# Kernel tuning notes

Hardware: AMD Instinct MI355X
Metric: run time of the kernel (lower is better)

## Reference

```python
import jax, jax.numpy as jnp
import numpy as np

jax.config.update("jax_enable_x64", True)  # FixedPointMul math is done in float64, as in torch

B, S, H = 8, 4096, 768


def setup_inputs():
    key = jax.random.key(0)
    k = jax.random.split(key, 6)
    s_act = jnp.array([4.0 / 127.0], dtype=jnp.float32)  # per-tensor 8-bit activation scale

    def qact(kk):  # produce int8-quantized-looking activations
        x = jax.random.normal(kk, (B, S, H), jnp.float32)
        return s_act * jnp.clip(jnp.round(x / s_act), -128, 127)

    return {
        "hidden_states": qact(k[0]),
        "hidden_states_scaling_factor": s_act,
        "input_tensor": qact(k[1]),
        "input_tensor_scaling_factor": s_act,
        "dense_weight": 0.02 * jax.random.normal(k[2], (H, H), jnp.float32),
        "dense_bias": 0.01 * jax.random.normal(k[3], (H,), jnp.float32),
        "ln_weight": 1.0 + 0.05 * jax.random.normal(k[4], (H,), jnp.float32),
        "ln_bias": 0.05 * jax.random.normal(k[5], (H,), jnp.float32),
    }


def _sym_scale(k, smin, smax):
    n = 2 ** (k - 1) - 1
    return jnp.clip(jnp.maximum(jnp.abs(smin), jnp.abs(smax)), 1e-8, None) / n


def _sym_quant(x, k, scale):
    n = 2 ** (k - 1) - 1
    return jnp.clip(jnp.round(x / scale), -n, n - 1)


def _batch_frexp(x):
    # returns (round(mantissa * 2^31), 31 - exponent) as in ibert batch_frexp
    m, e = jnp.frexp(x)
    return jnp.floor(m * (2.0 ** 31) + 0.5), 31.0 - e


def _fixedpoint_mul(x, pre_scale, bit, z_scale, identity=None, id_scale=None):
    n = 2 ** (bit - 1) - 1
    ps = jnp.reshape(pre_scale, (1, 1, -1)).astype(jnp.float64)
    z = z_scale.astype(jnp.float64)
    z_int = jnp.round(x.astype(jnp.float64) / ps)
    m, e = _batch_frexp(ps / z)
    out = jnp.round(z_int * m / (2.0 ** e))
    if identity is not None:
        isf = jnp.reshape(id_scale, (1, 1, -1)).astype(jnp.float64)
        wx = jnp.round(identity.astype(jnp.float64) / isf)
        m1, e1 = _batch_frexp(isf / z)
        out = out + jnp.round(wx * m1 / (2.0 ** e1))
    return jnp.clip(out, -n - 1, n).astype(jnp.float32)


def _quant_act(x, bit, pre_scale, identity=None, id_scale=None):
    x_act = x if identity is None else x + identity
    s = _sym_scale(bit, x_act.min(), x_act.max())  # per-tensor scale (dynamic range)
    q = _fixedpoint_mul(x, pre_scale, bit, s, identity, id_scale)
    return q * s, s


def reference(hidden_states, hidden_states_scaling_factor, input_tensor, input_tensor_scaling_factor, dense_weight, dense_bias, ln_weight, ln_bias):
    # ---- QuantLinear: per-channel int8 weights, int32 bias ----
    w_min = dense_weight.min(axis=1)
    w_max = dense_weight.max(axis=1)
    fc_scale = _sym_scale(8, w_min, w_max)                      # [H_out]
    w_int = _sym_quant(dense_weight, 8, fc_scale[:, None])      # [H_out, H_in]
    bias_scale = fc_scale * hidden_states_scaling_factor        # [H_out]
    b_int = _sym_quant(dense_bias, 32, bias_scale)
    x_int = hidden_states / hidden_states_scaling_factor
    hs = (jnp.einsum("bsh,oh->bso", x_int, w_int) + b_int) * bias_scale
    # dropout: eval mode -> identity
    # ---- QuantAct(22-bit) with quantized residual add ----
    hs, ln_in_scale = _quant_act(hs, 22, bias_scale, input_tensor, input_tensor_scaling_factor)
    # ---- IntLayerNorm (integer-only LayerNorm) ----
    x_int = hs / ln_in_scale
    mean_int = jnp.round(jnp.mean(x_int, axis=2, keepdims=True))
    y_int = x_int - mean_int
    var0 = jnp.sum(y_int ** 2, axis=2, keepdims=True)
    shift = jnp.ceil(jnp.log2(jnp.sqrt(jnp.maximum(var0, 1.0) / 2.0 ** 32)))  # set_shift (max_bit=32)
    shift = jnp.maximum(0.0, shift.max())
    y_sh = jnp.floor(y_int / 2.0 ** shift)
    var_int = jnp.sum(y_sh ** 2, axis=2, keepdims=True)
    std_int = jnp.floor(jnp.sqrt(var_int)) * 2.0 ** shift
    factor = jnp.floor(2.0 ** 31 / std_int)
    y_int = jnp.floor(y_int * factor / 2.0)
    sf = jnp.sqrt(jnp.float32(H)) / 2.0 ** 30
    bias_int = jnp.floor((ln_bias / ln_weight) / sf)
    y_int = y_int + bias_int
    sf_out = sf * ln_weight                                     # [H]
    hs = y_int * sf_out
    # ---- QuantAct(8-bit) output requantization ----
    hs, out_scale = _quant_act(hs, 8, sf_out)
    return hs, out_scale
```

## Files before the change

kernel.cpp:

```cpp
#include <hip/hip_runtime.h>

typedef int   v4i   __attribute__((ext_vector_type(4)));
typedef unsigned long u64x2 __attribute__((ext_vector_type(2)));

#define HDIM 768
#define NTOK 32768

static constexpr size_t WX_OFF   = 0;
static constexpr size_t WINT_OFF = 25165824;
static constexpr size_t FACT_OFF = WINT_OFF + 589824;
static constexpr size_t RS1_OFF  = WINT_OFF + 1179648;
static constexpr size_t RS2_OFF  = RS1_OFF + 6144;
static constexpr size_t BS_OFF   = RS2_OFF + 6144;
static constexpr size_t BINT_OFF = BS_OFF + 3072;
static constexpr size_t LNBI_OFF = BINT_OFF + 3072;
static constexpr size_t SFO_OFF  = LNBI_OFF + 3072;
static constexpr size_t SC_OFF   = SFO_OFF + 3072;
static constexpr size_t RSM1_OFF = SC_OFF + 64;
static constexpr size_t INP8_OFF = RSM1_OFF + 64;
static constexpr size_t WS_NEED8 = INP8_OFF + (size_t)NTOK * HDIM;

__device__ __forceinline__ unsigned fenc(float f) {
    unsigned u = __float_as_uint(f);
    return (u >> 31) ? ~u : (u | 0x80000000u);
}
__device__ __forceinline__ float fdec(unsigned e) {
    unsigned u = (e >> 31) ? (e & 0x7fffffffu) : ~e;
    return __uint_as_float(u);
}

#define GLDS16(g, l) __builtin_amdgcn_global_load_lds( \
    (const __attribute__((address_space(1))) unsigned int*)(g), \
    (__attribute__((address_space(3))) unsigned int*)(l), 16, 0, 0)

__device__ __forceinline__ int swz4(int r) { return (r & 3) ^ ((r >> 2) & 3); }

__global__ __launch_bounds__(256) void k0_prep(const float* __restrict__ W,
                                               const float* __restrict__ bias,
                                               const float* __restrict__ ln_w,
                                               const float* __restrict__ ln_b,
                                               const float* __restrict__ phsf,
                                               char* __restrict__ ws) {
    int o = blockIdx.x, tid = threadIdx.x;
    __shared__ float red[256];
    __shared__ float fc_sh;
    float m = 0.f;
    for (int j = tid; j < HDIM; j += 256) m = fmaxf(m, fabsf(W[(size_t)o * HDIM + j]));
    red[tid] = m;
    __syncthreads();
    for (int s = 128; s; s >>= 1) { if (tid < s) red[tid] = fmaxf(red[tid], red[tid + s]); __syncthreads(); }
    if (tid == 0) {
        float fc = fmaxf(red[0], 1e-8f) / 127.0f;
        float hsf = *phsf;
        float bs = fc * hsf;
        fc_sh = fc;
        ((float*)(ws + BS_OFF))[o] = bs;
        ((int*)(ws + BINT_OFF))[o] = (int)rintf(bias[o] / bs);
        float sf = sqrtf(768.0f) / 1073741824.0f;
        float lw = ln_w[o], lb = ln_b[o];
        ((int*)(ws + LNBI_OFF))[o] = (int)floorf((lb / lw) / sf);
        ((float*)(ws + SFO_OFF))[o] = sf * lw;
    }
    __syncthreads();
    float fc = fc_sh;
    char* w8 = (char*)(ws + WINT_OFF);
    for (int j = tid; j < HDIM; j += 256) {
        float q = rintf(W[(size_t)o * HDIM + j] / fc);
        q = fminf(fmaxf(q, -127.f), 126.f);
        w8[(size_t)o * HDIM + j] = (char)q;
    }
    if (blockIdx.x == 0 && tid < 8) {
        unsigned* sc = (unsigned*)(ws + SC_OFF);
        unsigned v = 0u;
        if (tid == 0 || tid == 2) v = 0xFFFFFFFFu;
        sc[tid] = v;
    }
}

__global__ __launch_bounds__(256) void kp_a8(const float* __restrict__ hs,
                                             const float* __restrict__ phsf,
                                             char* __restrict__ ws) {
    int tid = threadIdx.x;
    size_t b4 = (size_t)blockIdx.x * 1024 + tid;
    float inv = 1.0f / *phsf;
    const float4* in4 = (const float4*)hs;
    unsigned* o32 = (unsigned*)(ws + WX_OFF);
    #pragma unroll
    for (int j = 0; j < 4; ++j) {
        float4 v = in4[b4 + j * 256];
        int q0 = (int)rintf(v.x * inv), q1 = (int)rintf(v.y * inv);
        int q2 = (int)rintf(v.z * inv), q3 = (int)rintf(v.w * inv);
        o32[b4 + j * 256] = (unsigned)(q0 & 255) | ((unsigned)(q1 & 255) << 8) |
                            ((unsigned)(q2 & 255) << 16) | ((unsigned)(q3 & 255) << 24);
    }
}

__global__ __launch_bounds__(256) void kp_i8(const float* __restrict__ inp,
                                             const float* __restrict__ pisf,
                                             char* __restrict__ ws) {
    int tid = threadIdx.x;
    size_t b4 = (size_t)blockIdx.x * 1024 + tid;
    float inv = 1.0f / *pisf;
    const float4* in4 = (const float4*)inp;
    unsigned* o32 = (unsigned*)(ws + INP8_OFF);
    #pragma unroll
    for (int j = 0; j < 4; ++j) {
        float4 v = in4[b4 + j * 256];
        int q0 = (int)rintf(v.x * inv), q1 = (int)rintf(v.y * inv);
        int q2 = (int)rintf(v.z * inv), q3 = (int)rintf(v.w * inv);
        o32[b4 + j * 256] = (unsigned)(q0 & 255) | ((unsigned)(q1 & 255) << 8) |
                            ((unsigned)(q2 & 255) << 16) | ((unsigned)(q3 & 255) << 24);
    }
}

#define BM 128
#define BN 128
#define BK 64
#define NKT (HDIM / BK)
#define SROW 132
template<int U8>
__global__ __launch_bounds__(256, 3) void k1_gemm(const float* __restrict__ inp,
                                                  const char* __restrict__ i8,
                                                  const float* __restrict__ pisf,
                                                  char* __restrict__ ws,
                                                  int* __restrict__ accOut) {
    __shared__ alignas(16) char smem[32800];
    char* As0 = smem;
    char* Bs0 = smem + 16384;
    float* rmn = (float*)(smem + 32768);
    float* rmx = rmn + 4;
    int tid = threadIdx.x, lane = tid & 63, wave = tid >> 6;
    int wrow = lane & 15, g = lane >> 4;
    int bid = blockIdx.x;
    int xcd = bid & 7, slot = bid >> 3;
    int mtile = xcd * 32 + slot / 6;
    int ntile = slot % 6;
    int t0 = mtile * BM, o0 = ntile * BN;
    const char* a8 = (const char*)(ws + WX_OFF);
    const char* w8 = (const char*)(ws + WINT_OFF);

    const char* asrc[2]; const char* bsrc[2];
    int ldso[2];
    #pragma unroll
    for (int i = 0; i < 2; ++i) {
        int c = i * 256 + tid, r = c >> 2, s = c & 3;
        asrc[i] = a8 + (size_t)(t0 + r) * HDIM + (s ^ swz4(r)) * 16;
        bsrc[i] = w8 + (size_t)(o0 + r) * HDIM + (s ^ swz4(r)) * 16;
        ldso[i] = (i * 256 + wave * 64) * 16;
    }

    int wm = wave & 1, wn = wave >> 1;
    int aofs[4], bofs[4];
    #pragma unroll
    for (int mi = 0; mi < 4; ++mi) { int r = wm * 64 + mi * 16 + wrow; aofs[mi] = r * BK + ((g ^ swz4(r)) * 16); }
    #pragma unroll
    for (int nf = 0; nf < 4; ++nf) { int r = wn * 64 + nf * 16 + wrow; bofs[nf] = r * BK + ((g ^ swz4(r)) * 16); }

    #pragma unroll
    for (int i = 0; i < 2; ++i) GLDS16(asrc[i], As0 + ldso[i]);
    #pragma unroll
    for (int i = 0; i < 2; ++i) GLDS16(bsrc[i], Bs0 + ldso[i]);
    #pragma unroll
    for (int i = 0; i < 2; ++i) GLDS16(asrc[i] + BK, As0 + 8192 + ldso[i]);
    #pragma unroll
    for (int i = 0; i < 2; ++i) GLDS16(bsrc[i] + BK, Bs0 + 8192 + ldso[i]);
    asm volatile("s_waitcnt vmcnt(4)" ::: "memory");
    __builtin_amdgcn_s_barrier();

    v4i acc[4][4] = {};
    for (int kt = 0; kt < NKT; ++kt) {
        int cur = kt & 1;
        const char* Ac = As0 + cur * 8192;
        const char* Bc = Bs0 + cur * 8192;
        u64x2 af[4], bf[4];
        #pragma unroll
        for (int mi = 0; mi < 4; ++mi) af[mi] = *(const u64x2*)(Ac + aofs[mi]);
        #pragma unroll
        for (int nf = 0; nf < 4; ++nf) bf[nf] = *(const u64x2*)(Bc + bofs[nf]);
        asm volatile("s_waitcnt lgkmcnt(0)" ::: "memory");
        __builtin_amdgcn_s_barrier();
        if (kt + 2 < NKT) {
            #pragma unroll
            for (int i = 0; i < 2; ++i) GLDS16(asrc[i] + (kt + 2) * BK, As0 + cur * 8192 + ldso[i]);
            #pragma unroll
            for (int i = 0; i < 2; ++i) GLDS16(bsrc[i] + (kt + 2) * BK, Bs0 + cur * 8192 + ldso[i]);
        }
        __builtin_amdgcn_s_setprio(1);
        #pragma unroll
        for (int mi = 0; mi < 4; ++mi)
            #pragma unroll
            for (int nf = 0; nf < 4; ++nf) {
                acc[mi][nf] = __builtin_amdgcn_mfma_i32_16x16x32_i8((long)af[mi][0], (long)bf[nf][0], acc[mi][nf], 0, 0, 0);
                acc[mi][nf] = __builtin_amdgcn_mfma_i32_16x16x32_i8((long)af[mi][1], (long)bf[nf][1], acc[mi][nf], 0, 0, 0);
            }
        __builtin_amdgcn_s_setprio(0);
        if (kt + 2 < NKT) {
            asm volatile("s_waitcnt vmcnt(4)" ::: "memory");
            __builtin_amdgcn_s_barrier();
        } else if (kt + 2 == NKT) {
            asm volatile("s_waitcnt vmcnt(0)" ::: "memory");
            __builtin_amdgcn_s_barrier();
        }
    }

    const float* bscale = (const float*)(ws + BS_OFF);
    const int* bint = (const int*)(ws + BINT_OFF);
    float isf = U8 ? *pisf : 0.f;
    int* sAcc = (int*)smem;
    float lmn = 3.402823466e38f, lmx = -3.402823466e38f;
    #pragma unroll
    for (int mi = 0; mi < 4; ++mi) {
        __syncthreads();
        #pragma unroll
        for (int nf = 0; nf < 4; ++nf)
            #pragma unroll
            for (int r = 0; r < 4; ++r)
                sAcc[(wm * 16 + g * 4 + r) * SROW + wn * 64 + nf * 16 + wrow] = acc[mi][nf][r];
        __syncthreads();
        #pragma unroll
        for (int k = 0; k < 4; ++k) {
            int i4 = tid + k * 256;
            int sr = i4 >> 5, c4 = i4 & 31;
            int t = t0 + (sr >> 4) * 64 + mi * 16 + (sr & 15);
            int col = o0 + c4 * 4;
            int4 a4 = *(const int4*)&sAcc[sr * SROW + c4 * 4];
            int4 b4 = *(const int4*)&bint[col];
            float4 bs4 = *(const float4*)&bscale[col];
            a4.x += b4.x; a4.y += b4.y; a4.z += b4.z; a4.w += b4.w;
            size_t idx = (size_t)t * HDIM + col;
            *(int4*)&accOut[idx] = a4;
            float x0, x1, x2, x3;
            if (U8) {
                unsigned w = *(const unsigned*)(i8 + idx);
                x0 = (float)(int)(char)(w) * isf;
                x1 = (float)(int)(char)(w >> 8) * isf;
                x2 = (float)(int)(char)(w >> 16) * isf;
                x3 = (float)(int)(char)(w >> 24) * isf;
            } else {
                float4 x4 = *(const float4*)&inp[idx];
                x0 = x4.x; x1 = x4.y; x2 = x4.z; x3 = x4.w;
            }
            float xa;
            xa = (float)a4.x * bs4.x + x0; lmn = fminf(lmn, xa); lmx = fmaxf(lmx, xa);
            xa = (float)a4.y * bs4.y + x1; lmn = fminf(lmn, xa); lmx = fmaxf(lmx, xa);
            xa = (float)a4.z * bs4.z + x2; lmn = fminf(lmn, xa); lmx = fmaxf(lmx, xa);
            xa = (float)a4.w * bs4.w + x3; lmn = fminf(lmn, xa); lmx = fmaxf(lmx, xa);
        }
    }
    #pragma unroll
    for (int off = 32; off; off >>= 1) {
        lmn = fminf(lmn, __shfl_down(lmn, off));
        lmx = fmaxf(lmx, __shfl_down(lmx, off));
    }
    __syncthreads();
    if (lane == 0) { rmn[wave] = lmn; rmx[wave] = lmx; }
    __syncthreads();
    if (tid == 0) {
        float mn = fminf(fminf(rmn[0], rmn[1]), fminf(rmn[2], rmn[3]));
        float mx = fmaxf(fmaxf(rmx[0], rmx[1]), fmaxf(rmx[2], rmx[3]));
        volatile unsigned* sc = (volatile unsigned*)(ws + SC_OFF);
        unsigned emn = fenc(mn), emx = fenc(mx);
        if (emn < sc[0]) atomicMin((unsigned*)&sc[0], emn);
        if (emx > sc[1]) atomicMax((unsigned*)&sc[1], emx);
    }
}

__global__ __launch_bounds__(256) void k2_scale1(const float* __restrict__ pisf, char* __restrict__ ws) {
    __shared__ float s_sh;
    unsigned* sc = (unsigned*)(ws + SC_OFF);
    if (threadIdx.x == 0) {
        float mn = fdec(sc[0]), mx = fdec(sc[1]);
        float s = fmaxf(fmaxf(fabsf(mn), fabsf(mx)), 1e-8f) / 2097151.0f;
        ((float*)sc)[5] = s;
        s_sh = s;
        double r = (double)(*pisf) / (double)s;
        int ex; double mant = frexp(r, &ex);
        double m1 = floor(mant * 2147483648.0 + 0.5);
        ((double*)(ws + RSM1_OFF))[0] = m1 * exp2((double)(ex - 31));
    }
    __syncthreads();
    float s = s_sh;
    const float* bs = (const float*)(ws + BS_OFF);
    double* rs1 = (double*)(ws + RS1_OFF);
    for (int o = threadIdx.x; o < HDIM; o += 256) {
        double r = (double)bs[o] / (double)s;
        int ex; double mant = frexp(r, &ex);
        double m = floor(mant * 2147483648.0 + 0.5);
        rs1[o] = m * exp2((double)(ex - 31));
    }
}

template<int U8>
__global__ __launch_bounds__(256) void k3_rows(char* __restrict__ ws, int* __restrict__ buf,
                                               const float* __restrict__ inp,
                                               const char* __restrict__ i8,
                                               const float* __restrict__ pisf) {
    int tid = threadIdx.x, lane = tid & 63, wave = tid >> 6;
    int wid = blockIdx.x * 4 + wave;
    const double* rs1 = (const double*)(ws + RS1_OFF);
    double rsm1 = *(const double*)(ws + RSM1_OFF);
    float inv_isf = 1.0f / *pisf;
    double t_rs1[12];
    #pragma unroll
    for (int c = 0; c < 3; ++c) {
        int o0 = (lane + 64 * c) * 4;
        #pragma unroll
        for (int j = 0; j < 4; ++j) t_rs1[c * 4 + j] = rs1[o0 + j];
    }
    int localShift = 0;
    int4 aP[3]; float4 xP[3]; int wP[3];
    {
        size_t b0 = (size_t)(wid * 4) * HDIM;
        #pragma unroll
        for (int c = 0; c < 3; ++c) {
            aP[c] = ((const int4*)(buf + b0))[lane + 64 * c];
            if (U8) wP[c] = ((const int*)(i8 + b0))[lane + 64 * c];
            else    xP[c] = ((const float4*)(inp + b0))[lane + 64 * c];
        }
    }
    for (int rr = 0; rr < 4; ++rr) {
        int4 aN[3]; float4 xN[3]; int wN[3];
        if (rr < 3) {
            size_t nb = (size_t)(wid * 4 + rr + 1) * HDIM;
            #pragma unroll
            for (int c = 0; c < 3; ++c) {
                aN[c] = ((const int4*)(buf + nb))[lane + 64 * c];
                if (U8) wN[c] = ((const int*)(i8 + nb))[lane + 64 * c];
                else    xN[c] = ((const float4*)(inp + nb))[lane + 64 * c];
            }
        }
        size_t base = (size_t)(wid * 4 + rr) * HDIM;
        int q[12];
        int sum = 0;
        #pragma unroll
        for (int c = 0; c < 3; ++c) {
            int av[4] = {aP[c].x, aP[c].y, aP[c].z, aP[c].w};
            #pragma unroll
            for (int j = 0; j < 4; ++j) {
                double q1 = rint((double)av[j] * t_rs1[c * 4 + j]);
                int wxj;
                if (U8) wxj = (int)(char)(wP[c] >> (8 * j));
                else {
                    float xv = (j == 0) ? xP[c].x : (j == 1) ? xP[c].y : (j == 2) ? xP[c].z : xP[c].w;
                    wxj = (int)rintf(xv * inv_isf);
                }
                double qq = q1 + rint((double)wxj * rsm1);
                qq = fmin(fmax(qq, -2097152.0), 2097151.0);
                q[c * 4 + j] = (int)qq;
                sum += q[c * 4 + j];
            }
        }
        #pragma unroll
        for (int off = 32; off; off >>= 1) sum += __shfl_xor(sum, off);
        int mean = (int)rint((double)sum / 768.0);
        long long var0 = 0;
        #pragma unroll
        for (int k = 0; k < 12; ++k) { q[k] -= mean; var0 += (long long)q[k] * (long long)q[k]; }
        #pragma unroll
        for (int off = 32; off; off >>= 1) var0 += __shfl_xor(var0, off);
        #pragma unroll
        for (int c = 0; c < 3; ++c) {
            int4 y = {q[c * 4 + 0], q[c * 4 + 1], q[c * 4 + 2], q[c * 4 + 3]};
            ((int4*)(buf + base))[lane + 64 * c] = y;
        }
        if (lane == 0) {
            double v = (double)(var0 < 1 ? 1LL : var0);
            int sr = (int)ceil(0.5 * log2(v) - 16.0);
            localShift = max(localShift, sr);
        }
        #pragma unroll
        for (int c = 0; c < 3; ++c) { aP[c] = aN[c]; xP[c] = xN[c]; wP[c] = wN[c]; }
    }
    if (lane == 0 && localShift > 0) {
        int* sp = (int*)(ws + SC_OFF) + 4;
        if (localShift > *(volatile int*)sp) atomicMax(sp, localShift);
    }
}

__global__ __launch_bounds__(256) void k4_rows(char* __restrict__ ws, const int* __restrict__ buf) {
    int tid = threadIdx.x, lane = tid & 63, wave = tid >> 6;
    int wid = blockIdx.x * 4 + wave;
    int shift = *(((const int*)(ws + SC_OFF)) + 4);
    const int* lnbi = (const int*)(ws + LNBI_OFF);
    const float* sfo = (const float*)(ws + SFO_OFF);
    __shared__ float rmn[4], rmx[4];
    int t_lnbi[12]; float t_sfo[12];
    #pragma unroll
    for (int c = 0; c < 3; ++c) {
        int o0 = (lane + 64 * c) * 4;
        #pragma unroll
        for (int j = 0; j < 4; ++j) { t_lnbi[c * 4 + j] = lnbi[o0 + j]; t_sfo[c * 4 + j] = sfo[o0 + j]; }
    }
    unsigned* fact = (unsigned*)(ws + FACT_OFF);
    float lmn = 3.402823466e38f, lmx = -3.402823466e38f;
    int4 yP[3];
    {
        size_t b0 = (size_t)(wid * 4) * HDIM;
        #pragma unroll
        for (int c = 0; c < 3; ++c) yP[c] = ((const int4*)(buf + b0))[lane + 64 * c];
    }
    for (int rr = 0; rr < 4; ++rr) {
        int4 yN[3];
        if (rr < 3) {
            size_t nb = (size_t)(wid * 4 + rr + 1) * HDIM;
            #pragma unroll
            for (int c = 0; c < 3; ++c) yN[c] = ((const int4*)(buf + nb))[lane + 64 * c];
        }
        int yv[12];
        #pragma unroll
        for (int c = 0; c < 3; ++c) {
            yv[c * 4 + 0] = yP[c].x; yv[c * 4 + 1] = yP[c].y; yv[c * 4 + 2] = yP[c].z; yv[c * 4 + 3] = yP[c].w;
        }
        long long var = 0;
        #pragma unroll
        for (int k = 0; k < 12; ++k) { int ysh = yv[k] >> shift; var += (long long)ysh * (long long)ysh; }
        #pragma unroll
        for (int off = 32; off; off >>= 1) var += __shfl_xor(var, off);
        double std_int = floor(sqrt((double)var)) * (double)(1LL << shift);
        if (std_int < 1.0) std_int = 1.0;
        long long factor = (long long)floor(2147483648.0 / std_int);
        if (lane == 0) fact[wid * 4 + rr] = (unsigned)factor;
        #pragma unroll
        for (int k = 0; k < 12; ++k) {
            long long t = ((long long)yv[k] * factor) >> 1;
            int v2 = (int)t + t_lnbi[k];
            float h = (float)v2 * t_sfo[k];
            lmn = fminf(lmn, h);
            lmx = fmaxf(lmx, h);
        }
        #pragma unroll
        for (int c = 0; c < 3; ++c) yP[c] = yN[c];
    }
    #pragma unroll
    for (int off = 32; off; off >>= 1) {
        lmn = fminf(lmn, __shfl_xor(lmn, off));
        lmx = fmaxf(lmx, __shfl_xor(lmx, off));
    }
    if (lane == 0) { rmn[wave] = lmn; rmx[wave] = lmx; }
    __syncthreads();
    if (tid == 0) {
        float mn = fminf(fminf(rmn[0], rmn[1]), fminf(rmn[2], rmn[3]));
        float mx = fmaxf(fmaxf(rmx[0], rmx[1]), fmaxf(rmx[2], rmx[3]));
        volatile unsigned* sc = (volatile unsigned*)(ws + SC_OFF);
        unsigned emn = fenc(mn), emx = fenc(mx);
        if (emn < sc[2]) atomicMin((unsigned*)&sc[2], emn);
        if (emx > sc[3]) atomicMax((unsigned*)&sc[3], emx);
    }
}

__global__ __launch_bounds__(256) void k5_scale2(char* __restrict__ ws) {
    __shared__ float s_sh;
    unsigned* sc = (unsigned*)(ws + SC_OFF);
    if (threadIdx.x == 0) {
        float mn = fdec(sc[2]), mx = fdec(sc[3]);
        float s2 = fmaxf(fmaxf(fabsf(mn), fabsf(mx)), 1e-8f) / 127.0f;
        ((float*)sc)[6] = s2;
        s_sh = s2;
    }
    __syncthreads();
    float s2 = s_sh;
    const float* sfo = (const float*)(ws + SFO_OFF);
    double* rs2 = (double*)(ws + RS2_OFF);
    for (int o = threadIdx.x; o < HDIM; o += 256) {
        double r = (double)sfo[o] / (double)s2;
        int ex; double mant = frexp(r, &ex);
        double m = floor(mant * 2147483648.0 + 0.5);
        rs2[o] = m * exp2((double)(ex - 31));
    }
}

__global__ __launch_bounds__(256) void k6_out(char* __restrict__ ws, float* __restrict__ out) {
    int tid = threadIdx.x, lane = tid & 63, wave = tid >> 6;
    int wid = blockIdx.x * 4 + wave;
    const double* rs2 = (const double*)(ws + RS2_OFF);
    const int* lnbi = (const int*)(ws + LNBI_OFF);
    const unsigned* fact = (const unsigned*)(ws + FACT_OFF);
    float s2 = ((const float*)(ws + SC_OFF))[6];
    double t_rs2[12]; int t_lnbi[12];
    #pragma unroll
    for (int c = 0; c < 3; ++c) {
        int o0 = (lane + 64 * c) * 4;
        #pragma unroll
        for (int j = 0; j < 4; ++j) { t_rs2[c * 4 + j] = rs2[o0 + j]; t_lnbi[c * 4 + j] = lnbi[o0 + j]; }
    }
    int* buf = (int*)out;
    int4 yP[3];
    {
        size_t b0 = (size_t)(wid * 4) * HDIM;
        #pragma unroll
        for (int c = 0; c < 3; ++c) yP[c] = ((const int4*)(buf + b0))[lane + 64 * c];
    }
    for (int rr = 0; rr < 4; ++rr) {
        int4 yN[3];
        if (rr < 3) {
            size_t nb = (size_t)(wid * 4 + rr + 1) * HDIM;
            #pragma unroll
            for (int c = 0; c < 3; ++c) yN[c] = ((const int4*)(buf + nb))[lane + 64 * c];
        }
        size_t base = (size_t)(wid * 4 + rr) * HDIM;
        long long factor = (long long)fact[wid * 4 + rr];
        int yv[12];
        #pragma unroll
        for (int c = 0; c < 3; ++c) {
            yv[c * 4 + 0] = yP[c].x; yv[c * 4 + 1] = yP[c].y; yv[c * 4 + 2] = yP[c].z; yv[c * 4 + 3] = yP[c].w;
        }
        #pragma unroll
        for (int c = 0; c < 3; ++c) {
            float4 r;
            float* rp = &r.x;
            #pragma unroll
            for (int j = 0; j < 4; ++j) {
                int k = c * 4 + j;
                long long t = ((long long)yv[k] * factor) >> 1;
                int v2 = (int)t + t_lnbi[k];
                double q = rint((double)v2 * t_rs2[k]);
                q = fmin(fmax(q, -128.0), 127.0);
                rp[j] = (float)q * s2;
            }
            ((float4*)(out + base))[lane + 64 * c] = r;
        }
        #pragma unroll
        for (int c = 0; c < 3; ++c) yP[c] = yN[c];
    }
    if (wid == 0 && tid == 0) out[(size_t)NTOK * HDIM] = s2;
}

extern "C" void kernel_launch(void* const* d_in, const int* in_sizes, int n_in,
                              void* d_out, int out_size, void* d_ws, size_t ws_size,
                              hipStream_t stream) {
    const float* hs   = (const float*)d_in[0];
    const float* phsf = (const float*)d_in[1];
    const float* inp  = (const float*)d_in[2];
    const float* pisf = (const float*)d_in[3];
    const float* W    = (const float*)d_in[4];
    const float* bias = (const float*)d_in[5];
    const float* ln_w = (const float*)d_in[6];
    const float* ln_b = (const float*)d_in[7];
    char* ws = (char*)d_ws;
    float* out = (float*)d_out;
    int* buf = (int*)d_out;
    const char* i8 = (const char*)(ws + INP8_OFF);
    bool use8 = ws_size >= WS_NEED8;

    k0_prep<<<HDIM, 256, 0, stream>>>(W, bias, ln_w, ln_b, phsf, ws);
    kp_a8<<<NTOK * HDIM / 4096, 256, 0, stream>>>(hs, phsf, ws);
    if (use8) {
        kp_i8<<<NTOK * HDIM / 4096, 256, 0, stream>>>(inp, pisf, ws);
        k1_gemm<1><<<(NTOK / BM) * (HDIM / BN), 256, 0, stream>>>(inp, i8, pisf, ws, buf);
        k2_scale1<<<1, 256, 0, stream>>>(pisf, ws);
        k3_rows<1><<<NTOK / 16, 256, 0, stream>>>(ws, buf, inp, i8, pisf);
    } else {
        k1_gemm<0><<<(NTOK / BM) * (HDIM / BN), 256, 0, stream>>>(inp, i8, pisf, ws, buf);
        k2_scale1<<<1, 256, 0, stream>>>(pisf, ws);
        k3_rows<0><<<NTOK / 16, 256, 0, stream>>>(ws, buf, inp, i8, pisf);
    }
    k4_rows<<<NTOK / 16, 256, 0, stream>>>(ws, buf);
    k5_scale2<<<1, 256, 0, stream>>>(ws);
    k6_out<<<NTOK / 16, 256, 0, stream>>>(ws, out);
}
```

Baseline: 432.4 us.

## Fuse LayerNorm stats pass into residual kernel via speculative per-shift candidates

```diff
diff --git a/kernel.cpp b/kernel.cpp
--- a/kernel.cpp
+++ b/kernel.cpp
@@ -5,10 +5,10 @@
 
 #define HDIM 768
 #define NTOK 32768
+#define NCAND 12
 
 static constexpr size_t WX_OFF   = 0;
 static constexpr size_t WINT_OFF = 25165824;
-static constexpr size_t FACT_OFF = WINT_OFF + 589824;
 static constexpr size_t RS1_OFF  = WINT_OFF + 1179648;
 static constexpr size_t RS2_OFF  = RS1_OFF + 6144;
 static constexpr size_t BS_OFF   = RS2_OFF + 6144;
@@ -17,8 +17,9 @@
 static constexpr size_t SFO_OFF  = LNBI_OFF + 3072;
 static constexpr size_t SC_OFF   = SFO_OFF + 3072;
 static constexpr size_t RSM1_OFF = SC_OFF + 64;
-static constexpr size_t INP8_OFF = RSM1_OFF + 64;
-static constexpr size_t WS_NEED8 = INP8_OFF + (size_t)NTOK * HDIM;
+static constexpr size_t CMIN_OFF = SC_OFF + 128;
+static constexpr size_t CMAX_OFF = SC_OFF + 192;
+static constexpr size_t FCT_OFF  = SC_OFF + 256;
 
 __device__ __forceinline__ unsigned fenc(float f) {
     unsigned u = __float_as_uint(f);
@@ -69,11 +70,17 @@
         q = fminf(fmaxf(q, -127.f), 126.f);
         w8[(size_t)o * HDIM + j] = (char)q;
     }
-    if (blockIdx.x == 0 && tid < 8) {
-        unsigned* sc = (unsigned*)(ws + SC_OFF);
-        unsigned v = 0u;
-        if (tid == 0 || tid == 2) v = 0xFFFFFFFFu;
-        sc[tid] = v;
+    if (blockIdx.x == 0) {
+        if (tid < 8) {
+            unsigned* sc = (unsigned*)(ws + SC_OFF);
+            unsigned v = 0u;
+            if (tid == 0 || tid == 2) v = 0xFFFFFFFFu;
+            sc[tid] = v;
+        }
+        if (tid < 16) {
+            ((unsigned*)(ws + CMIN_OFF))[tid] = 0xFFFFFFFFu;
+            ((unsigned*)(ws + CMAX_OFF))[tid] = 0u;
+        }
     }
 }
 
@@ -95,33 +102,12 @@
     }
 }
 
-__global__ __launch_bounds__(256) void kp_i8(const float* __restrict__ inp,
-                                             const float* __restrict__ pisf,
-                                             char* __restrict__ ws) {
-    int tid = threadIdx.x;
-    size_t b4 = (size_t)blockIdx.x * 1024 + tid;
-    float inv = 1.0f / *pisf;
-    const float4* in4 = (const float4*)inp;
-    unsigned* o32 = (unsigned*)(ws + INP8_OFF);
-    #pragma unroll
-    for (int j = 0; j < 4; ++j) {
-        float4 v = in4[b4 + j * 256];
-        int q0 = (int)rintf(v.x * inv), q1 = (int)rintf(v.y * inv);
-        int q2 = (int)rintf(v.z * inv), q3 = (int)rintf(v.w * inv);
-        o32[b4 + j * 256] = (unsigned)(q0 & 255) | ((unsigned)(q1 & 255) << 8) |
-                            ((unsigned)(q2 & 255) << 16) | ((unsigned)(q3 & 255) << 24);
-    }
-}
-
 #define BM 128
 #define BN 128
 #define BK 64
 #define NKT (HDIM / BK)
 #define SROW 132
-template<int U8>
 __global__ __launch_bounds__(256, 3) void k1_gemm(const float* __restrict__ inp,
-                                                  const char* __restrict__ i8,
-                                                  const float* __restrict__ pisf,
                                                   char* __restrict__ ws,
                                                   int* __restrict__ accOut) {
     __shared__ alignas(16) char smem[32800];
@@ -205,7 +191,6 @@
 
     const float* bscale = (const float*)(ws + BS_OFF);
     const int* bint = (const int*)(ws + BINT_OFF);
-    float isf = U8 ? *pisf : 0.f;
     int* sAcc = (int*)smem;
     float lmn = 3.402823466e38f, lmx = -3.402823466e38f;
     #pragma unroll
@@ -229,22 +214,12 @@
             a4.x += b4.x; a4.y += b4.y; a4.z += b4.z; a4.w += b4.w;
             size_t idx = (size_t)t * HDIM + col;
             *(int4*)&accOut[idx] = a4;
-            float x0, x1, x2, x3;
-            if (U8) {
-                unsigned w = *(const unsigned*)(i8 + idx);
-                x0 = (float)(int)(char)(w) * isf;
-                x1 = (float)(int)(char)(w >> 8) * isf;
-                x2 = (float)(int)(char)(w >> 16) * isf;
-                x3 = (float)(int)(char)(w >> 24) * isf;
-            } else {
-                float4 x4 = *(const float4*)&inp[idx];
-                x0 = x4.x; x1 = x4.y; x2 = x4.z; x3 = x4.w;
-            }
+            float4 x4 = *(const float4*)&inp[idx];
             float xa;
-            xa = (float)a4.x * bs4.x + x0; lmn = fminf(lmn, xa); lmx = fmaxf(lmx, xa);
-            xa = (float)a4.y * bs4.y + x1; lmn = fminf(lmn, xa); lmx = fmaxf(lmx, xa);
-            xa = (float)a4.z * bs4.z + x2; lmn = fminf(lmn, xa); lmx = fmaxf(lmx, xa);
-            xa = (float)a4.w * bs4.w + x3; lmn = fminf(lmn, xa); lmx = fmaxf(lmx, xa);
+            xa = (float)a4.x * bs4.x + x4.x; lmn = fminf(lmn, xa); lmx = fmaxf(lmx, xa);
+            xa = (float)a4.y * bs4.y + x4.y; lmn = fminf(lmn, xa); lmx = fmaxf(lmx, xa);
+            xa = (float)a4.z * bs4.z + x4.z; lmn = fminf(lmn, xa); lmx = fmaxf(lmx, xa);
+            xa = (float)a4.w * bs4.w + x4.w; lmn = fminf(lmn, xa); lmx = fmaxf(lmx, xa);
         }
     }
     #pragma unroll
@@ -290,43 +265,50 @@
     }
 }
 
-template<int U8>
-__global__ __launch_bounds__(256) void k3_rows(char* __restrict__ ws, int* __restrict__ buf,
-                                               const float* __restrict__ inp,
-                                               const char* __restrict__ i8,
-                                               const float* __restrict__ pisf) {
+__global__ __launch_bounds__(256) void k3f(char* __restrict__ ws, int* __restrict__ buf,
+                                           const float* __restrict__ inp,
+                                           const float* __restrict__ pisf) {
     int tid = threadIdx.x, lane = tid & 63, wave = tid >> 6;
     int wid = blockIdx.x * 4 + wave;
     const double* rs1 = (const double*)(ws + RS1_OFF);
     double rsm1 = *(const double*)(ws + RSM1_OFF);
     float inv_isf = 1.0f / *pisf;
-    double t_rs1[12];
+    const int* lnbi = (const int*)(ws + LNBI_OFF);
+    const float* sfo = (const float*)(ws + SFO_OFF);
+    unsigned* fct = (unsigned*)(ws + FCT_OFF);
+    __shared__ float smn[4][NCAND], smx[4][NCAND];
+    double t_rs1[12]; int t_lnbi[12]; float t_sfo[12];
     #pragma unroll
     for (int c = 0; c < 3; ++c) {
         int o0 = (lane + 64 * c) * 4;
         #pragma unroll
-        for (int j = 0; j < 4; ++j) t_rs1[c * 4 + j] = rs1[o0 + j];
+        for (int j = 0; j < 4; ++j) {
+            t_rs1[c * 4 + j] = rs1[o0 + j];
+            t_lnbi[c * 4 + j] = lnbi[o0 + j];
+            t_sfo[c * 4 + j] = sfo[o0 + j];
+        }
     }
     int localShift = 0;
-    int4 aP[3]; float4 xP[3]; int wP[3];
+    float cmn[NCAND], cmx[NCAND];
+    #pragma unroll
+    for (int s = 0; s < NCAND; ++s) { cmn[s] = 3.402823466e38f; cmx[s] = -3.402823466e38f; }
+    int4 aP[3]; float4 xP[3];
     {
         size_t b0 = (size_t)(wid * 4) * HDIM;
         #pragma unroll
         for (int c = 0; c < 3; ++c) {
             aP[c] = ((const int4*)(buf + b0))[lane + 64 * c];
-            if (U8) wP[c] = ((const int*)(i8 + b0))[lane + 64 * c];
-            else    xP[c] = ((const float4*)(inp + b0))[lane + 64 * c];
+            xP[c] = ((const float4*)(inp + b0))[lane + 64 * c];
         }
     }
     for (int rr = 0; rr < 4; ++rr) {
-        int4 aN[3]; float4 xN[3]; int wN[3];
+        int4 aN[3]; float4 xN[3];
         if (rr < 3) {
             size_t nb = (size_t)(wid * 4 + rr + 1) * HDIM;
             #pragma unroll
             for (int c = 0; c < 3; ++c) {
                 aN[c] = ((const int4*)(buf + nb))[lane + 64 * c];
-                if (U8) wN[c] = ((const int*)(i8 + nb))[lane + 64 * c];
-                else    xN[c] = ((const float4*)(inp + nb))[lane + 64 * c];
+                xN[c] = ((const float4*)(inp + nb))[lane + 64 * c];
             }
         }
         size_t base = (size_t)(wid * 4 + rr) * HDIM;
@@ -335,15 +317,11 @@
         #pragma unroll
         for (int c = 0; c < 3; ++c) {
             int av[4] = {aP[c].x, aP[c].y, aP[c].z, aP[c].w};
+            float xv[4] = {xP[c].x, xP[c].y, xP[c].z, xP[c].w};
             #pragma unroll
             for (int j = 0; j < 4; ++j) {
                 double q1 = rint((double)av[j] * t_rs1[c * 4 + j]);
-                int wxj;
-                if (U8) wxj = (int)(char)(wP[c] >> (8 * j));
-                else {
-                    float xv = (j == 0) ? xP[c].x : (j == 1) ? xP[c].y : (j == 2) ? xP[c].z : xP[c].w;
-                    wxj = (int)rintf(xv * inv_isf);
-                }
+                int wxj = (int)rintf(xv[j] * inv_isf);
                 double qq = q1 + rint((double)wxj * rsm1);
                 qq = fmin(fmax(qq, -2097152.0), 2097151.0);
                 q[c * 4 + j] = (int)qq;
@@ -353,108 +331,92 @@
         #pragma unroll
         for (int off = 32; off; off >>= 1) sum += __shfl_xor(sum, off);
         int mean = (int)rint((double)sum / 768.0);
-        long long var0 = 0;
-        #pragma unroll
-        for (int k = 0; k < 12; ++k) { q[k] -= mean; var0 += (long long)q[k] * (long long)q[k]; }
-        #pragma unroll
-        for (int off = 32; off; off >>= 1) var0 += __shfl_xor(var0, off);
+        long long v0 = 0;
+        #pragma unroll
+        for (int k = 0; k < 12; ++k) { q[k] -= mean; v0 += (long long)q[k] * (long long)q[k]; }
+        #pragma unroll
+        for (int off = 32; off; off >>= 1) v0 += __shfl_xor(v0, off);
         #pragma unroll
         for (int c = 0; c < 3; ++c) {
             int4 y = {q[c * 4 + 0], q[c * 4 + 1], q[c * 4 + 2], q[c * 4 + 3]};
             ((int4*)(buf + base))[lane + 64 * c] = y;
         }
-        if (lane == 0) {
-            double v = (double)(var0 < 1 ? 1LL : var0);
-            int sr = (int)ceil(0.5 * log2(v) - 16.0);
-            localShift = max(localShift, sr);
-        }
-        #pragma unroll
-        for (int c = 0; c < 3; ++c) { aP[c] = aN[c]; xP[c] = xN[c]; wP[c] = wN[c]; }
+        double vd = (double)(v0 < 1 ? 1LL : v0);
+        int sr = (int)ceil(0.5 * log2(vd) - 16.0);
+        if (sr < 0) sr = 0;
+        localShift = max(localShift, sr);
+        #pragma unroll
+        for (int s = 0; s < NCAND; ++s) {
+            if (s >= sr) {
+                long long vs;
+                if (s == 0) vs = v0;
+                else {
+                    vs = 0;
+                    #pragma unroll
+                    for (int k = 0; k < 12; ++k) { int t = q[k] >> s; vs += (long long)t * (long long)t; }
+                    #pragma unroll
+                    for (int off = 32; off; off >>= 1) vs += __shfl_xor(vs, off);
+                }
+                double std_int = floor(sqrt((double)vs)) * (double)(1 << s);
+                if (std_int < 1.0) std_int = 1.0;
+                long long factor = (long long)floor(2147483648.0 / std_int);
+                if (lane == 0) fct[(size_t)(wid * 4 + rr) * 16 + s] = (unsigned)factor;
+                #pragma unroll
+                for (int k = 0; k < 12; ++k) {
+                    long long t = ((long long)q[k] * factor) >> 1;
+                    int v2 = (int)t + t_lnbi[k];
+                    float h = (float)v2 * t_sfo[k];
+                    cmn[s] = fminf(cmn[s], h);
+                    cmx[s] = fmaxf(cmx[s], h);
+                }
+            }
+        }
+        #pragma unroll
+        for (int c = 0; c < 3; ++c) { aP[c] = aN[c]; xP[c] = xN[c]; }
     }
     if (lane == 0 && localShift > 0) {
         int* sp = (int*)(ws + SC_OFF) + 4;
         if (localShift > *(volatile int*)sp) atomicMax(sp, localShift);
     }
-}
-
-__global__ __launch_bounds__(256) void k4_rows(char* __restrict__ ws, const int* __restrict__ buf) {
-    int tid = threadIdx.x, lane = tid & 63, wave = tid >> 6;
-    int wid = blockIdx.x * 4 + wave;
-    int shift = *(((const int*)(ws + SC_OFF)) + 4);
-    const int* lnbi = (const int*)(ws + LNBI_OFF);
-    const float* sfo = (const float*)(ws + SFO_OFF);
-    __shared__ float rmn[4], rmx[4];
-    int t_lnbi[12]; float t_sfo[12];
-    #pragma unroll
-    for (int c = 0; c < 3; ++c) {
-        int o0 = (lane + 64 * c) * 4;
-        #pragma unroll
-        for (int j = 0; j < 4; ++j) { t_lnbi[c * 4 + j] = lnbi[o0 + j]; t_sfo[c * 4 + j] = sfo[o0 + j]; }
-    }
-    unsigned* fact = (unsigned*)(ws + FACT_OFF);
-    float lmn = 3.402823466e38f, lmx = -3.402823466e38f;
-    int4 yP[3];
-    {
-        size_t b0 = (size_t)(wid * 4) * HDIM;
-        #pragma unroll
-        for (int c = 0; c < 3; ++c) yP[c] = ((const int4*)(buf + b0))[lane + 64 * c];
-    }
-    for (int rr = 0; rr < 4; ++rr) {
-        int4 yN[3];
-        if (rr < 3) {
-            size_t nb = (size_t)(wid * 4 + rr + 1) * HDIM;
-            #pragma unroll
-            for (int c = 0; c < 3; ++c) yN[c] = ((const int4*)(buf + nb))[lane + 64 * c];
-        }
-        int yv[12];
-        #pragma unroll
-        for (int c = 0; c < 3; ++c) {
-            yv[c * 4 + 0] = yP[c].x; yv[c * 4 + 1] = yP[c].y; yv[c * 4 + 2] = yP[c].z; yv[c * 4 + 3] = yP[c].w;
-        }
-        long long var = 0;
-        #pragma unroll
-        for (int k = 0; k < 12; ++k) { int ysh = yv[k] >> shift; var += (long long)ysh * (long long)ysh; }
-        #pragma unroll
-        for (int off = 32; off; off >>= 1) var += __shfl_xor(var, off);
-        double std_int = floor(sqrt((double)var)) * (double)(1LL << shift);
-        if (std_int < 1.0) std_int = 1.0;
-        long long factor = (long long)floor(2147483648.0 / std_int);
-        if (lane == 0) fact[wid * 4 + rr] = (unsigned)factor;
-        #pragma unroll
-        for (int k = 0; k < 12; ++k) {
-            long long t = ((long long)yv[k] * factor) >> 1;
-            int v2 = (int)t + t_lnbi[k];
-            float h = (float)v2 * t_sfo[k];
-            lmn = fminf(lmn, h);
-            lmx = fmaxf(lmx, h);
-        }
-        #pragma unroll
-        for (int c = 0; c < 3; ++c) yP[c] = yN[c];
-    }
-    #pragma unroll
-    for (int off = 32; off; off >>= 1) {
-        lmn = fminf(lmn, __shfl_xor(lmn, off));
-        lmx = fmaxf(lmx, __shfl_xor(lmx, off));
-    }
-    if (lane == 0) { rmn[wave] = lmn; rmx[wave] = lmx; }
-    __syncthreads();
-    if (tid == 0) {
-        float mn = fminf(fminf(rmn[0], rmn[1]), fminf(rmn[2], rmn[3]));
-        float mx = fmaxf(fmaxf(rmx[0], rmx[1]), fmaxf(rmx[2], rmx[3]));
-        volatile unsigned* sc = (volatile unsigned*)(ws + SC_OFF);
-        unsigned emn = fenc(mn), emx = fenc(mx);
-        if (emn < sc[2]) atomicMin((unsigned*)&sc[2], emn);
-        if (emx > sc[3]) atomicMax((unsigned*)&sc[3], emx);
+    #pragma unroll
+    for (int s = 0; s < NCAND; ++s) {
+        #pragma unroll
+        for (int off = 32; off; off >>= 1) {
+            cmn[s] = fminf(cmn[s], __shfl_xor(cmn[s], off));
+            cmx[s] = fmaxf(cmx[s], __shfl_xor(cmx[s], off));
+        }
+    }
+    if (lane == 0) {
+        #pragma unroll
+        for (int s = 0; s < NCAND; ++s) { smn[wave][s] = cmn[s]; smx[wave][s] = cmx[s]; }
+    }
+    __syncthreads();
+    if (tid < NCAND) {
+        float m = fminf(fminf(smn[0][tid], smn[1][tid]), fminf(smn[2][tid], smn[3][tid]));
+        if (m < 3.3e38f) {
+            volatile unsigned* cm = (volatile unsigned*)(ws + CMIN_OFF);
+            unsigned e = fenc(m);
+            if (e < cm[tid]) atomicMin((unsigned*)&cm[tid], e);
+        }
+    } else if (tid >= 64 && tid < 64 + NCAND) {
+        int s = tid - 64;
+        float m = fmaxf(fmaxf(smx[0][s], smx[1][s]), fmaxf(smx[2][s], smx[3][s]));
+        if (m > -3.3e38f) {
+            volatile unsigned* cm = (volatile unsigned*)(ws + CMAX_OFF);
+            unsigned e = fenc(m);
+            if (e > cm[s]) atomicMax((unsigned*)&cm[s], e);
+        }
     }
 }
 
 __global__ __launch_bounds__(256) void k5_scale2(char* __restrict__ ws) {
     __shared__ float s_sh;
-    unsigned* sc = (unsigned*)(ws + SC_OFF);
     if (threadIdx.x == 0) {
-        float mn = fdec(sc[2]), mx = fdec(sc[3]);
+        int shift = ((const int*)(ws + SC_OFF))[4];
+        float mn = fdec(((const unsigned*)(ws + CMIN_OFF))[shift]);
+        float mx = fdec(((const unsigned*)(ws + CMAX_OFF))[shift]);
         float s2 = fmaxf(fmaxf(fabsf(mn), fabsf(mx)), 1e-8f) / 127.0f;
-        ((float*)sc)[6] = s2;
+        ((float*)(ws + SC_OFF))[6] = s2;
         s_sh = s2;
     }
     __syncthreads();
@@ -474,7 +436,8 @@
     int wid = blockIdx.x * 4 + wave;
     const double* rs2 = (const double*)(ws + RS2_OFF);
     const int* lnbi = (const int*)(ws + LNBI_OFF);
-    const unsigned* fact = (const unsigned*)(ws + FACT_OFF);
+    const unsigned* fct = (const unsigned*)(ws + FCT_OFF);
+    int shift = ((const int*)(ws + SC_OFF))[4];
     float s2 = ((const float*)(ws + SC_OFF))[6];
     double t_rs2[12]; int t_lnbi[12];
     #pragma unroll
@@ -498,7 +461,7 @@
             for (int c = 0; c < 3; ++c) yN[c] = ((const int4*)(buf + nb))[lane + 64 * c];
         }
         size_t base = (size_t)(wid * 4 + rr) * HDIM;
-        long long factor = (long long)fact[wid * 4 + rr];
+        long long factor = (long long)fct[(size_t)(wid * 4 + rr) * 16 + shift];
         int yv[12];
         #pragma unroll
         for (int c = 0; c < 3; ++c) {
@@ -539,22 +502,12 @@
     char* ws = (char*)d_ws;
     float* out = (float*)d_out;
     int* buf = (int*)d_out;
-    const char* i8 = (const char*)(ws + INP8_OFF);
-    bool use8 = ws_size >= WS_NEED8;
 
     k0_prep<<<HDIM, 256, 0, stream>>>(W, bias, ln_w, ln_b, phsf, ws);
     kp_a8<<<NTOK * HDIM / 4096, 256, 0, stream>>>(hs, phsf, ws);
-    if (use8) {
-        kp_i8<<<NTOK * HDIM / 4096, 256, 0, stream>>>(inp, pisf, ws);
-        k1_gemm<1><<<(NTOK / BM) * (HDIM / BN), 256, 0, stream>>>(inp, i8, pisf, ws, buf);
-        k2_scale1<<<1, 256, 0, stream>>>(pisf, ws);
-        k3_rows<1><<<NTOK / 16, 256, 0, stream>>>(ws, buf, inp, i8, pisf);
-    } else {
-        k1_gemm<0><<<(NTOK / BM) * (HDIM / BN), 256, 0, stream>>>(inp, i8, pisf, ws, buf);
-        k2_scale1<<<1, 256, 0, stream>>>(pisf, ws);
-        k3_rows<0><<<NTOK / 16, 256, 0, stream>>>(ws, buf, inp, i8, pisf);
-    }
-    k4_rows<<<NTOK / 16, 256, 0, stream>>>(ws, buf);
+    k1_gemm<<<(NTOK / BM) * (HDIM / BN), 256, 0, stream>>>(inp, ws, buf);
+    k2_scale1<<<1, 256, 0, stream>>>(pisf, ws);
+    k3f<<<NTOK / 16, 256, 0, stream>>>(ws, buf, inp, pisf);
     k5_scale2<<<1, 256, 0, stream>>>(ws);
     k6_out<<<NTOK / 16, 256, 0, stream>>>(ws, out);
 }
```

After: 422.9 us. 2.2% less time.
